# Kernel optimization log

Measured on AMD Instinct MI355X. Metric: run time of the kernel, lower is better.

Reference implementation:

```python
import jax, jax.numpy as jnp
import numpy as np

N = 100000      # nodes
E = 1600000     # edges (avg degree 16)
NF = 1          # node_feature_dim
EF = 1          # edge_feature_dim
H = 64          # hidden_dim
L = 5           # num_layers


def _linear_init(key, fan_in, fan_out):
    # torch nn.Linear default: U(-1/sqrt(fan_in), 1/sqrt(fan_in)) for W and b
    s = 1.0 / np.sqrt(fan_in)
    kw, kb = jax.random.split(key)
    w = jax.random.uniform(kw, (fan_in, fan_out), minval=-s, maxval=s, dtype=jnp.float32)
    b = jax.random.uniform(kb, (fan_out,), minval=-s, maxval=s, dtype=jnp.float32)
    return w, b


def setup_inputs() -> dict:
    key = jax.random.key(0)
    ks = jax.random.split(key, 8)
    x = jax.random.normal(ks[0], (N, NF), dtype=jnp.float32)
    edge_index = jax.random.randint(ks[1], (2, E), 0, N, dtype=jnp.int32)
    edge_attr = jax.random.uniform(ks[2], (E, EF), dtype=jnp.float32)

    emb_w, emb_b = _linear_init(ks[3], NF, H)
    fc_w, fc_b = _linear_init(ks[4], H, 1)

    msg_w1, msg_b1, msg_w2, msg_b2 = [], [], [], []
    upd_w1, upd_b1, upd_w2, upd_b2 = [], [], [], []
    lk = jax.random.split(ks[5], L)
    for l in range(L):
        k1, k2, k3, k4 = jax.random.split(lk[l], 4)
        w, b = _linear_init(k1, H + EF, H); msg_w1.append(w); msg_b1.append(b)
        w, b = _linear_init(k2, H, H);      msg_w2.append(w); msg_b2.append(b)
        w, b = _linear_init(k3, 2 * H, H);  upd_w1.append(w); upd_b1.append(b)
        w, b = _linear_init(k4, H, H);      upd_w2.append(w); upd_b2.append(b)

    stack = lambda xs: jnp.stack(xs, axis=0)
    return {
        "x": x, "edge_index": edge_index, "edge_attr": edge_attr,
        "emb_w": emb_w, "emb_b": emb_b,
        "msg_w1": stack(msg_w1), "msg_b1": stack(msg_b1),
        "msg_w2": stack(msg_w2), "msg_b2": stack(msg_b2),
        "upd_w1": stack(upd_w1), "upd_b1": stack(upd_b1),
        "upd_w2": stack(upd_w2), "upd_b2": stack(upd_b2),
        "fc_w": fc_w, "fc_b": fc_b,
    }


def reference(x, edge_index, edge_attr, emb_w, emb_b,
              msg_w1, msg_b1, msg_w2, msg_b2,
              upd_w1, upd_b1, upd_w2, upd_b2, fc_w, fc_b):
    src = edge_index[0]  # x_j (source)
    dst = edge_index[1]  # aggregation target i
    n = x.shape[0]

    h = x @ emb_w + emb_b  # [N, H]
    for l in range(msg_w1.shape[0]):
        # message: MLP(cat[x_j, edge_attr])
        m = jnp.concatenate([h[src], edge_attr], axis=1)  # [E, H+EF]
        m = jax.nn.relu(m @ msg_w1[l] + msg_b1[l]) @ msg_w2[l] + msg_b2[l]  # [E, H]
        # scatter-min aggregate; torch_scatter fills empty segments with 0
        aggr = jax.ops.segment_min(m, dst, num_segments=n)
        aggr = jnp.where(jnp.isfinite(aggr), aggr, jnp.zeros_like(aggr))
        # update: MLP(cat[x, aggr])
        u = jnp.concatenate([h, aggr], axis=1)  # [N, 2H]
        h = jax.nn.relu(u @ upd_w1[l] + upd_b1[l]) @ upd_w2[l] + upd_b2[l]
    return (h @ fc_w + fc_b).squeeze(-1)  # [N]
```

## Files before the change

kernel.cpp:

```cpp
#include <hip/hip_runtime.h>
#include <math.h>

#define N_NODES 100000
#define N_EDGES 1600000
#define HDIM 64
#define SCAN_T 1024
#define SCAN_CHUNK 98
#define NPB 64
#define LBLOCKS 1563
#define BSTRIDE 66

__device__ __forceinline__ unsigned encMin(float f) {
  unsigned u = __float_as_uint(f);
  return (u & 0x80000000u) ? ~u : (u | 0x80000000u);
}
__device__ __forceinline__ float decMin(unsigned u) {
  unsigned b = (u & 0x80000000u) ? (u & 0x7FFFFFFFu) : ~u;
  return __uint_as_float(b);
}


__global__ __launch_bounds__(256) void k_zero_int(int* __restrict__ p, int n) {
  int i = blockIdx.x * 256 + threadIdx.x;
  if (i < n) p[i] = 0;
}

__global__ __launch_bounds__(256) void k_deg_count(const int* __restrict__ ei,
                                                   int* __restrict__ deg) {
  int e = blockIdx.x * 256 + threadIdx.x;
  if (e < N_EDGES) atomicAdd(&deg[ei[N_EDGES + e]], 1);
}

__global__ __launch_bounds__(SCAN_T) void k_rowptr(const int* __restrict__ deg,
                                                   int* __restrict__ row_ptr) {
  __shared__ int sums[SCAN_T];
  const int t = threadIdx.x;
  const int lo = t * SCAN_CHUNK;
  const int hi = min(lo + SCAN_CHUNK, N_NODES);
  int s = 0;
  for (int i = lo; i < hi; ++i) s += deg[i];
  sums[t] = s;
  __syncthreads();
  for (int off = 1; off < SCAN_T; off <<= 1) {
    int v = (t >= off) ? sums[t - off] : 0;
    __syncthreads();
    sums[t] += v;
    __syncthreads();
  }
  int run = (t == 0) ? 0 : sums[t - 1];
  for (int i = lo; i < hi; ++i) { row_ptr[i] = run; run += deg[i]; }
  if (t == SCAN_T - 1) row_ptr[N_NODES] = run;
}

__global__ __launch_bounds__(256) void k_scatter(
    const int* __restrict__ ei, const float* __restrict__ eattr,
    const int* __restrict__ row_ptr, int* __restrict__ cursor,
    int* __restrict__ s_src, float* __restrict__ s_ea, int* __restrict__ s_dl) {
  int e = blockIdx.x * 256 + threadIdx.x;
  if (e >= N_EDGES) return;
  int d = ei[N_EDGES + e];
  int pos = row_ptr[d] + atomicAdd(&cursor[d], 1);
  s_src[pos] = ei[e];
  s_ea[pos] = eattr[e];
  s_dl[pos] = d & (NPB - 1);
}


__global__ __launch_bounds__(256) void k_embed_z(
    const float* __restrict__ x, const float* __restrict__ emb_w,
    const float* __restrict__ emb_b,
    const float* __restrict__ w1, const float* __restrict__ b1,
    float* __restrict__ h, float* __restrict__ z) {
  __shared__ float hs[64][65];
  const int t = threadIdx.x;
  const int nl = t >> 2;
  const int l4 = t & 3;
  const int i = blockIdx.x * 64 + nl;
  const bool valid = (i < N_NODES);
  const int jbase = l4 * 16;
  const float xv = valid ? x[i] : 0.0f;

  float hv[16];
  #pragma unroll
  for (int jj = 0; jj < 16; ++jj) {
    int j = jbase + jj;
    hv[jj] = fmaf(xv, emb_w[j], emb_b[j]);
    hs[nl][j] = hv[jj];
  }
  if (valid) {
    #pragma unroll
    for (int q = 0; q < 4; ++q)
      reinterpret_cast<float4*>(h + (size_t)i * HDIM)[l4 * 4 + q] =
          make_float4(hv[4*q], hv[4*q+1], hv[4*q+2], hv[4*q+3]);
  }
  __syncthreads();

  float acc[16];
  #pragma unroll
  for (int jj = 0; jj < 16; ++jj) acc[jj] = b1[jbase + jj];
  #pragma unroll 8
  for (int k = 0; k < 64; ++k) {
    float hk = hs[nl][k];
    const float* wr = w1 + k * 64 + jbase;
    #pragma unroll
    for (int jj = 0; jj < 16; ++jj) acc[jj] = fmaf(hk, wr[jj], acc[jj]);
  }
  if (valid) {
    #pragma unroll
    for (int q = 0; q < 4; ++q)
      reinterpret_cast<float4*>(z + (size_t)i * HDIM)[l4 * 4 + q] =
          make_float4(acc[4*q], acc[4*q+1], acc[4*q+2], acc[4*q+3]);
  }
}

template <int LAST>
__global__ __launch_bounds__(256) void k_layer(
    const int* __restrict__ row_ptr,
    const int* __restrict__ s_src, const float* __restrict__ s_ea,
    const int* __restrict__ s_dl,
    const float* __restrict__ z_in,
    const float* __restrict__ w1b, const float* __restrict__ w2,
    const float* __restrict__ b2,
    const float* __restrict__ u1w, const float* __restrict__ u1b,
    const float* __restrict__ u2w, const float* __restrict__ u2b,
    const float* __restrict__ w1next, const float* __restrict__ b1next,
    const float* __restrict__ fcw, const float* __restrict__ fcb,
    float* __restrict__ h, float* __restrict__ z_out, float* __restrict__ out) {
  __shared__ float buf[2][64][BSTRIDE];
  __shared__ unsigned acc_u[NPB][65];
  __shared__ float ps[NPB][4];
  float* acc_f = (float*)acc_u;

  const int t = threadIdx.x;
  const int lane = t & 63;
  const int w = __builtin_amdgcn_readfirstlane(t >> 6);
  const int pair = w >> 1;
  const int wi = w & 1;
  const int nbase = blockIdx.x * NPB;

  for (int i = t; i < NPB * 65; i += 256) ((unsigned*)acc_u)[i] = 0xFFFFFFFFu;

  const int eb0 = row_ptr[nbase];
  const int eb1 = row_ptr[min(nbase + NPB, N_NODES)];
  const int n = eb1 - eb0;
  const int emid = eb0 + (n >> 1);
  const int p0 = pair ? emid : eb0;
  const int p1 = pair ? eb1 : emid;
  const int nbat = ((n - (n >> 1)) + 63) >> 6;

  const int rq = lane >> 3;
  const int q  = lane & 7;
  const float4 w1bA = ((const float4*)w1b)[q];
  const float4 w1bB = ((const float4*)w1b)[q + 8];
  const int jb = wi * 32;

  __syncthreads();

  for (int bi = 0; bi < nbat; ++bi) {
    const int base = p0 + (bi << 6);
    const int cnt  = min(64, p1 - base);

    if (cnt > 0) {
      #pragma unroll
      for (int i = 0; i < 4; ++i) {
        const int row = wi * 32 + i * 8 + rq;
        const int ed = base + row;
        const bool v = (row < cnt);
        const int src = v ? s_src[ed] : 0;
        const float ea = v ? s_ea[ed] : 0.0f;
        const float4* zr = (const float4*)(z_in + (size_t)src * HDIM);
        float4 a = zr[q];
        float4 b = zr[q + 8];
        float2 h0, h1, h2, h3;
        h0.x = fmaxf(fmaf(ea, w1bA.x, a.x), 0.f);
        h0.y = fmaxf(fmaf(ea, w1bA.y, a.y), 0.f);
        h1.x = fmaxf(fmaf(ea, w1bA.z, a.z), 0.f);
        h1.y = fmaxf(fmaf(ea, w1bA.w, a.w), 0.f);
        h2.x = fmaxf(fmaf(ea, w1bB.x, b.x), 0.f);
        h2.y = fmaxf(fmaf(ea, w1bB.y, b.y), 0.f);
        h3.x = fmaxf(fmaf(ea, w1bB.z, b.z), 0.f);
        h3.y = fmaxf(fmaf(ea, w1bB.w, b.w), 0.f);
        float* bp = &buf[pair][row][0];
        *(float2*)&bp[q * 4]          = h0;
        *(float2*)&bp[q * 4 + 2]      = h1;
        *(float2*)&bp[32 + q * 4]     = h2;
        *(float2*)&bp[32 + q * 4 + 2] = h3;
      }
    }
    __syncthreads();

    float m[32];
    if (cnt > 0) {
      #pragma unroll
      for (int c = 0; c < 32; ++c) m[c] = b2[jb + c];
      const float* bp = &buf[pair][lane][0];
      #pragma unroll 4
      for (int k2 = 0; k2 < 32; ++k2) {
        float2 hq = *(const float2*)&bp[k2 * 2];
        const float* wr0 = w2 + (2 * k2 + 0) * 64 + jb;
        const float* wr1 = w2 + (2 * k2 + 1) * 64 + jb;
        #pragma unroll
        for (int c = 0; c < 32; ++c) m[c] = fmaf(hq.x, wr0[c], m[c]);
        #pragma unroll
        for (int c = 0; c < 32; ++c) m[c] = fmaf(hq.y, wr1[c], m[c]);
      }
    }
    __syncthreads();

    if (cnt > 0) {
      float* bp = &buf[pair][lane][jb];
      #pragma unroll
      for (int c2 = 0; c2 < 16; ++c2)
        *(float2*)&bp[c2 * 2] = make_float2(m[2*c2], m[2*c2+1]);
    }
    __syncthreads();

    if (cnt > 0) {
      const int e0 = wi * 32;
      const int e1 = min(wi * 32 + 32, cnt);
      float run = INFINITY;
      int cur = -1;
      for (int e = e0; e < e1; ++e) {
        const int dl = s_dl[base + e];
        if (dl != cur) {
          if (cur >= 0) atomicMin(&acc_u[cur][lane], encMin(run));
          cur = dl; run = INFINITY;
        }
        run = fminf(run, buf[pair][e][lane]);
      }
      if (cur >= 0) atomicMin(&acc_u[cur][lane], encMin(run));
    }
    __syncthreads();
  }

  const int jq = w * 16;
  const int node = nbase + lane;
  const bool valid = (node < N_NODES);
  const size_t off = (size_t)(valid ? node : 0) * HDIM;

  #pragma unroll
  for (int j = 0; j < 16; ++j) {
    float f = decMin(acc_u[lane][jq + j]);
    if (!isfinite(f)) f = 0.f;
    acc_f[lane * 65 + jq + j] = f;
  }
  __syncthreads();

  float acc[16];
  #pragma unroll
  for (int j = 0; j < 16; ++j) acc[j] = u1b[jq + j];
  {
    const float4* hr = reinterpret_cast<const float4*>(h + off);
    for (int k4 = 0; k4 < 16; ++k4) {
      float4 uv = hr[k4];
      const float* w0 = u1w + (4*k4+0) * 64 + jq;
      const float* w1 = u1w + (4*k4+1) * 64 + jq;
      const float* w2r = u1w + (4*k4+2) * 64 + jq;
      const float* w3 = u1w + (4*k4+3) * 64 + jq;
      #pragma unroll
      for (int j = 0; j < 16; ++j) acc[j] = fmaf(uv.x, w0[j], acc[j]);
      #pragma unroll
      for (int j = 0; j < 16; ++j) acc[j] = fmaf(uv.y, w1[j], acc[j]);
      #pragma unroll
      for (int j = 0; j < 16; ++j) acc[j] = fmaf(uv.z, w2r[j], acc[j]);
      #pragma unroll
      for (int j = 0; j < 16; ++j) acc[j] = fmaf(uv.w, w3[j], acc[j]);
    }
    #pragma unroll 4
    for (int k = 0; k < 64; ++k) {
      float uk = acc_f[lane * 65 + k];
      const float* wr = u1w + (64 + k) * 64 + jq;
      #pragma unroll
      for (int j = 0; j < 16; ++j) acc[j] = fmaf(uk, wr[j], acc[j]);
    }
  }
  __syncthreads();
  #pragma unroll
  for (int j = 0; j < 16; ++j) acc_f[lane * 65 + jq + j] = fmaxf(acc[j], 0.f);
  __syncthreads();

  float hn[16];
  #pragma unroll
  for (int j = 0; j < 16; ++j) hn[j] = u2b[jq + j];
  #pragma unroll 4
  for (int k = 0; k < 64; ++k) {
    float hk = acc_f[lane * 65 + k];
    const float* wr = u2w + k * 64 + jq;
    #pragma unroll
    for (int j = 0; j < 16; ++j) hn[j] = fmaf(hk, wr[j], hn[j]);
  }
  if (valid) {
    #pragma unroll
    for (int v4 = 0; v4 < 4; ++v4)
      reinterpret_cast<float4*>(h + off)[w * 4 + v4] =
          make_float4(hn[4*v4], hn[4*v4+1], hn[4*v4+2], hn[4*v4+3]);
  }

  if (LAST) {
    float s = 0.0f;
    #pragma unroll
    for (int j = 0; j < 16; ++j) s = fmaf(hn[j], fcw[jq + j], s);
    ps[lane][w] = s;
    __syncthreads();
    if (w == 0 && valid)
      out[node] = ps[lane][0] + ps[lane][1] + ps[lane][2] + ps[lane][3] + fcb[0];
  } else {
    __syncthreads();
    #pragma unroll
    for (int j = 0; j < 16; ++j) acc_f[lane * 65 + jq + j] = hn[j];
    __syncthreads();
    float zz[16];
    #pragma unroll
    for (int j = 0; j < 16; ++j) zz[j] = b1next[jq + j];
    #pragma unroll 4
    for (int k = 0; k < 64; ++k) {
      float hk = acc_f[lane * 65 + k];
      const float* wr = w1next + k * 64 + jq;
      #pragma unroll
      for (int j = 0; j < 16; ++j) zz[j] = fmaf(hk, wr[j], zz[j]);
    }
    if (valid) {
      #pragma unroll
      for (int v4 = 0; v4 < 4; ++v4)
        reinterpret_cast<float4*>(z_out + off)[w * 4 + v4] =
            make_float4(zz[4*v4], zz[4*v4+1], zz[4*v4+2], zz[4*v4+3]);
    }
  }
}

extern "C" void kernel_launch(void* const* d_in, const int* in_sizes, int n_in,
                              void* d_out, int out_size, void* d_ws, size_t ws_size,
                              hipStream_t stream) {
  const float* x      = (const float*)d_in[0];
  const int*   ei     = (const int*)d_in[1];
  const float* eattr  = (const float*)d_in[2];
  const float* emb_w  = (const float*)d_in[3];
  const float* emb_b  = (const float*)d_in[4];
  const float* msg_w1 = (const float*)d_in[5];
  const float* msg_b1 = (const float*)d_in[6];
  const float* msg_w2 = (const float*)d_in[7];
  const float* msg_b2 = (const float*)d_in[8];
  const float* upd_w1 = (const float*)d_in[9];
  const float* upd_b1 = (const float*)d_in[10];
  const float* upd_w2 = (const float*)d_in[11];
  const float* upd_b2 = (const float*)d_in[12];
  const float* fc_w   = (const float*)d_in[13];
  const float* fc_b   = (const float*)d_in[14];
  float* out = (float*)d_out;

  float* h     = (float*)d_ws;
  float* zA    = h + (size_t)N_NODES * HDIM;
  float* zB    = zA + (size_t)N_NODES * HDIM;
  float* s_ea  = zB + (size_t)N_NODES * HDIM;
  int*   s_src = (int*)(s_ea + N_EDGES);
  int*   s_dl  = s_src + N_EDGES;
  int*   row_ptr = s_dl + N_EDGES;
  int*   deg   = row_ptr + (N_NODES + 1);
  int*   cursor= deg + N_NODES;

  const int nodeBlocks64 = (N_NODES + 63) / 64;
  const int edgeBlocks = (N_EDGES + 255) / 256;

  k_zero_int<<<(2 * N_NODES + 255) / 256, 256, 0, stream>>>(deg, 2 * N_NODES);
  k_deg_count<<<edgeBlocks, 256, 0, stream>>>(ei, deg);
  k_rowptr<<<1, SCAN_T, 0, stream>>>(deg, row_ptr);
  k_scatter<<<edgeBlocks, 256, 0, stream>>>(ei, eattr, row_ptr, cursor,
                                            s_src, s_ea, s_dl);

  k_embed_z<<<nodeBlocks64, 256, 0, stream>>>(x, emb_w, emb_b, msg_w1, msg_b1, h, zA);

  float* zin = zA;
  float* zout = zB;
  for (int l = 0; l < 5; ++l) {
    const float* w1b = msg_w1 + l * 65 * 64 + 64 * 64;
    const float* w2  = msg_w2 + l * 64 * 64;
    const float* b2  = msg_b2 + l * 64;
    const float* u1w = upd_w1 + l * 128 * 64;
    const float* u1b = upd_b1 + l * 64;
    const float* u2w = upd_w2 + l * 64 * 64;
    const float* u2b = upd_b2 + l * 64;
    if (l < 4) {
      k_layer<0><<<LBLOCKS, 256, 0, stream>>>(
          row_ptr, s_src, s_ea, s_dl, zin,
          w1b, w2, b2, u1w, u1b, u2w, u2b,
          msg_w1 + (l + 1) * 65 * 64, msg_b1 + (l + 1) * 64,
          nullptr, nullptr,
          h, zout, nullptr);
      float* tmp = zin; zin = zout; zout = tmp;
    } else {
      k_layer<1><<<LBLOCKS, 256, 0, stream>>>(
          row_ptr, s_src, s_ea, s_dl, zin,
          w1b, w2, b2, u1w, u1b, u2w, u2b,
          nullptr, nullptr,
          fc_w, fc_b,
          h, nullptr, out);
    }
  }
}
```

Before: 2.219 ms.

## Precompute per-source-node affine message coefficients with sparse ReLU-ambiguity correction

The per-edge 64x64 message MLP is replaced by a per-node precomputation. For each source node it builds C and D so that the message equals C + ea*D, assuming each hidden unit's ReLU state is fixed for edge_attr in [0,1]. Units whose sign can flip inside that range are listed per node and corrected per edge with a short loop. Per-edge work drops to a 512-byte gather plus a few corrections, at the cost of an extra build kernel per layer, a larger per-node CD buffer, and reliance on edge_attr lying in [0,1].

```diff
diff --git a/kernel.cpp b/kernel.cpp
--- a/kernel.cpp
+++ b/kernel.cpp
@@ -8,7 +8,6 @@
 #define SCAN_CHUNK 98
 #define NPB 64
 #define LBLOCKS 1563
-#define BSTRIDE 66
 
 __device__ __forceinline__ unsigned encMin(float f) {
   unsigned u = __float_as_uint(f);
@@ -55,78 +54,133 @@
 __global__ __launch_bounds__(256) void k_scatter(
     const int* __restrict__ ei, const float* __restrict__ eattr,
     const int* __restrict__ row_ptr, int* __restrict__ cursor,
-    int* __restrict__ s_src, float* __restrict__ s_ea, int* __restrict__ s_dl) {
+    int* __restrict__ s_sd, float* __restrict__ s_ea) {
   int e = blockIdx.x * 256 + threadIdx.x;
   if (e >= N_EDGES) return;
   int d = ei[N_EDGES + e];
   int pos = row_ptr[d] + atomicAdd(&cursor[d], 1);
-  s_src[pos] = ei[e];
+  s_sd[pos] = ei[e] | ((d & (NPB - 1)) << 20);
   s_ea[pos] = eattr[e];
-  s_dl[pos] = d & (NPB - 1);
-}
-
-
-__global__ __launch_bounds__(256) void k_embed_z(
-    const float* __restrict__ x, const float* __restrict__ emb_w,
-    const float* __restrict__ emb_b,
-    const float* __restrict__ w1, const float* __restrict__ b1,
-    float* __restrict__ h, float* __restrict__ z) {
+}
+
+
+__global__ __launch_bounds__(256) void k_embed(
+    const float* __restrict__ x, const float* __restrict__ ew,
+    const float* __restrict__ eb, float* __restrict__ h) {
+  int gid = blockIdx.x * 256 + threadIdx.x;
+  if (gid >= N_NODES * 16) return;
+  int node = gid >> 4;
+  int q = gid & 15;
+  float xv = x[node];
+  float4 w = ((const float4*)ew)[q];
+  float4 b = ((const float4*)eb)[q];
+  ((float4*)h)[gid] = make_float4(fmaf(xv, w.x, b.x), fmaf(xv, w.y, b.y),
+                                  fmaf(xv, w.z, b.z), fmaf(xv, w.w, b.w));
+}
+
+__global__ __launch_bounds__(256) void k_build(
+    const float* __restrict__ h,
+    const float* __restrict__ w1,
+    const float* __restrict__ b1,
+    const float* __restrict__ w2,
+    const float* __restrict__ b2,
+    float* __restrict__ z,
+    float* __restrict__ CD,
+    unsigned char* __restrict__ amb,
+    int* __restrict__ amb_cnt) {
   __shared__ float hs[64][65];
+  __shared__ float zs[64][65];
   const int t = threadIdx.x;
   const int nl = t >> 2;
   const int l4 = t & 3;
-  const int i = blockIdx.x * 64 + nl;
-  const bool valid = (i < N_NODES);
-  const int jbase = l4 * 16;
-  const float xv = valid ? x[i] : 0.0f;
-
-  float hv[16];
-  #pragma unroll
-  for (int jj = 0; jj < 16; ++jj) {
-    int j = jbase + jj;
-    hv[jj] = fmaf(xv, emb_w[j], emb_b[j]);
-    hs[nl][j] = hv[jj];
-  }
-  if (valid) {
-    #pragma unroll
-    for (int q = 0; q < 4; ++q)
-      reinterpret_cast<float4*>(h + (size_t)i * HDIM)[l4 * 4 + q] =
-          make_float4(hv[4*q], hv[4*q+1], hv[4*q+2], hv[4*q+3]);
-  }
-  __syncthreads();
-
-  float acc[16];
-  #pragma unroll
-  for (int jj = 0; jj < 16; ++jj) acc[jj] = b1[jbase + jj];
-  #pragma unroll 8
+  const int node = blockIdx.x * 64 + nl;
+  const bool valid = (node < N_NODES);
+  const size_t off = (size_t)(valid ? node : 0) * HDIM;
+  const int jb = l4 * 16;
+
+  #pragma unroll
+  for (int q = 0; q < 4; ++q) {
+    float4 hv = ((const float4*)(h + off))[l4 * 4 + q];
+    hs[nl][jb + 4*q + 0] = hv.x;
+    hs[nl][jb + 4*q + 1] = hv.y;
+    hs[nl][jb + 4*q + 2] = hv.z;
+    hs[nl][jb + 4*q + 3] = hv.w;
+  }
+  __syncthreads();
+
+  float zr[16];
+  #pragma unroll
+  for (int j = 0; j < 16; ++j) zr[j] = b1[jb + j];
+  #pragma unroll 4
   for (int k = 0; k < 64; ++k) {
     float hk = hs[nl][k];
-    const float* wr = w1 + k * 64 + jbase;
-    #pragma unroll
-    for (int jj = 0; jj < 16; ++jj) acc[jj] = fmaf(hk, wr[jj], acc[jj]);
-  }
+    const float* wr = w1 + k * 64 + jb;
+    #pragma unroll
+    for (int j = 0; j < 16; ++j) zr[j] = fmaf(hk, wr[j], zr[j]);
+  }
+  #pragma unroll
+  for (int j = 0; j < 16; ++j) zs[nl][jb + j] = zr[j];
   if (valid) {
     #pragma unroll
     for (int q = 0; q < 4; ++q)
-      reinterpret_cast<float4*>(z + (size_t)i * HDIM)[l4 * 4 + q] =
-          make_float4(acc[4*q], acc[4*q+1], acc[4*q+2], acc[4*q+3]);
+      ((float4*)(z + off))[l4 * 4 + q] =
+          make_float4(zr[4*q], zr[4*q+1], zr[4*q+2], zr[4*q+3]);
+  }
+  __syncthreads();
+
+  const float* w1b = w1 + 64 * 64;
+  float c[16], d[16];
+  #pragma unroll
+  for (int j = 0; j < 16; ++j) { c[j] = b2[jb + j]; d[j] = 0.0f; }
+  #pragma unroll 4
+  for (int k = 0; k < 64; ++k) {
+    float zk = zs[nl][k];
+    float vk = w1b[k];
+    float zv = zk + vk;
+    bool act = (fminf(zk, zv) >= 0.0f);
+    float cz = act ? zk : 0.0f;
+    float cv = act ? vk : 0.0f;
+    const float* wr = w2 + k * 64 + jb;
+    #pragma unroll
+    for (int j = 0; j < 16; ++j) {
+      c[j] = fmaf(cz, wr[j], c[j]);
+      d[j] = fmaf(cv, wr[j], d[j]);
+    }
+  }
+  if (valid) {
+    float4* cdp = (float4*)(CD + (size_t)node * 128);
+    #pragma unroll
+    for (int j2 = 0; j2 < 8; ++j2)
+      cdp[jb / 2 + j2] = make_float4(c[2*j2], d[2*j2], c[2*j2+1], d[2*j2+1]);
+  }
+
+  if (l4 == 0 && valid) {
+    int cnt = 0;
+    for (int k = 0; k < 64; ++k) {
+      float zk = zs[nl][k];
+      float vk = w1b[k];
+      float zv = zk + vk;
+      if (fminf(zk, zv) < 0.0f && fmaxf(zk, zv) > 0.0f) {
+        amb[(size_t)node * 64 + cnt] = (unsigned char)k;
+        ++cnt;
+      }
+    }
+    amb_cnt[node] = cnt;
   }
 }
 
 template <int LAST>
 __global__ __launch_bounds__(256) void k_layer(
     const int* __restrict__ row_ptr,
-    const int* __restrict__ s_src, const float* __restrict__ s_ea,
-    const int* __restrict__ s_dl,
-    const float* __restrict__ z_in,
+    const int* __restrict__ s_sd, const float* __restrict__ s_ea,
+    const float2* __restrict__ CDm,
+    const float* __restrict__ z,
     const float* __restrict__ w1b, const float* __restrict__ w2,
-    const float* __restrict__ b2,
+    const unsigned char* __restrict__ amb, const int* __restrict__ amb_cnt,
     const float* __restrict__ u1w, const float* __restrict__ u1b,
     const float* __restrict__ u2w, const float* __restrict__ u2b,
-    const float* __restrict__ w1next, const float* __restrict__ b1next,
     const float* __restrict__ fcw, const float* __restrict__ fcb,
-    float* __restrict__ h, float* __restrict__ z_out, float* __restrict__ out) {
-  __shared__ float buf[2][64][BSTRIDE];
+    float* __restrict__ h, float* __restrict__ out) {
   __shared__ unsigned acc_u[NPB][65];
   __shared__ float ps[NPB][4];
   float* acc_f = (float*)acc_u;
@@ -134,8 +188,6 @@
   const int t = threadIdx.x;
   const int lane = t & 63;
   const int w = __builtin_amdgcn_readfirstlane(t >> 6);
-  const int pair = w >> 1;
-  const int wi = w & 1;
   const int nbase = blockIdx.x * NPB;
 
   for (int i = t; i < NPB * 65; i += 256) ((unsigned*)acc_u)[i] = 0xFFFFFFFFu;
@@ -143,95 +195,48 @@
   const int eb0 = row_ptr[nbase];
   const int eb1 = row_ptr[min(nbase + NPB, N_NODES)];
   const int n = eb1 - eb0;
-  const int emid = eb0 + (n >> 1);
-  const int p0 = pair ? emid : eb0;
-  const int p1 = pair ? eb1 : emid;
-  const int nbat = ((n - (n >> 1)) + 63) >> 6;
-
-  const int rq = lane >> 3;
-  const int q  = lane & 7;
-  const float4 w1bA = ((const float4*)w1b)[q];
-  const float4 w1bB = ((const float4*)w1b)[q + 8];
-  const int jb = wi * 32;
-
-  __syncthreads();
-
-  for (int bi = 0; bi < nbat; ++bi) {
-    const int base = p0 + (bi << 6);
-    const int cnt  = min(64, p1 - base);
-
-    if (cnt > 0) {
-      #pragma unroll
-      for (int i = 0; i < 4; ++i) {
-        const int row = wi * 32 + i * 8 + rq;
-        const int ed = base + row;
-        const bool v = (row < cnt);
-        const int src = v ? s_src[ed] : 0;
-        const float ea = v ? s_ea[ed] : 0.0f;
-        const float4* zr = (const float4*)(z_in + (size_t)src * HDIM);
-        float4 a = zr[q];
-        float4 b = zr[q + 8];
-        float2 h0, h1, h2, h3;
-        h0.x = fmaxf(fmaf(ea, w1bA.x, a.x), 0.f);
-        h0.y = fmaxf(fmaf(ea, w1bA.y, a.y), 0.f);
-        h1.x = fmaxf(fmaf(ea, w1bA.z, a.z), 0.f);
-        h1.y = fmaxf(fmaf(ea, w1bA.w, a.w), 0.f);
-        h2.x = fmaxf(fmaf(ea, w1bB.x, b.x), 0.f);
-        h2.y = fmaxf(fmaf(ea, w1bB.y, b.y), 0.f);
-        h3.x = fmaxf(fmaf(ea, w1bB.z, b.z), 0.f);
-        h3.y = fmaxf(fmaf(ea, w1bB.w, b.w), 0.f);
-        float* bp = &buf[pair][row][0];
-        *(float2*)&bp[q * 4]          = h0;
-        *(float2*)&bp[q * 4 + 2]      = h1;
-        *(float2*)&bp[32 + q * 4]     = h2;
-        *(float2*)&bp[32 + q * 4 + 2] = h3;
+  const int we0 = eb0 + (n * w) / 4;
+  const int we1 = eb0 + (n * (w + 1)) / 4;
+  __syncthreads();
+
+  float run = INFINITY;
+  int cur = -1;
+  for (int e = we0; e < we1; e += 4) {
+    const int nb = min(4, we1 - e);
+    int sd[4]; float ea4[4]; float2 cd[4];
+    #pragma unroll
+    for (int i = 0; i < 4; ++i) {
+      sd[i] = (i < nb) ? s_sd[e + i] : 0;
+      ea4[i] = (i < nb) ? s_ea[e + i] : 0.0f;
+    }
+    #pragma unroll
+    for (int i = 0; i < 4; ++i)
+      cd[i] = CDm[(size_t)(sd[i] & 0xFFFFF) * 64 + lane];
+    #pragma unroll
+    for (int i = 0; i < 4; ++i) {
+      if (i >= nb) break;
+      const int src = sd[i] & 0xFFFFF;
+      const int dl = sd[i] >> 20;
+      float m = fmaf(ea4[i], cd[i].y, cd[i].x);
+      const int cnt = amb_cnt[src];
+      if (cnt) {
+        const unsigned char* ap = amb + (size_t)src * 64;
+        const float* zrow = z + (size_t)src * 64;
+        for (int a = 0; a < cnt; ++a) {
+          const int k = ap[a];
+          const float tt = fmaf(ea4[i], w1b[k], zrow[k]);
+          if (tt > 0.0f) m = fmaf(tt, w2[k * 64 + lane], m);
+        }
       }
-    }
-    __syncthreads();
-
-    float m[32];
-    if (cnt > 0) {
-      #pragma unroll
-      for (int c = 0; c < 32; ++c) m[c] = b2[jb + c];
-      const float* bp = &buf[pair][lane][0];
-      #pragma unroll 4
-      for (int k2 = 0; k2 < 32; ++k2) {
-        float2 hq = *(const float2*)&bp[k2 * 2];
-        const float* wr0 = w2 + (2 * k2 + 0) * 64 + jb;
-        const float* wr1 = w2 + (2 * k2 + 1) * 64 + jb;
-        #pragma unroll
-        for (int c = 0; c < 32; ++c) m[c] = fmaf(hq.x, wr0[c], m[c]);
-        #pragma unroll
-        for (int c = 0; c < 32; ++c) m[c] = fmaf(hq.y, wr1[c], m[c]);
+      if (dl != cur) {
+        if (cur >= 0) atomicMin(&acc_u[cur][lane], encMin(run));
+        cur = dl; run = INFINITY;
       }
-    }
-    __syncthreads();
-
-    if (cnt > 0) {
-      float* bp = &buf[pair][lane][jb];
-      #pragma unroll
-      for (int c2 = 0; c2 < 16; ++c2)
-        *(float2*)&bp[c2 * 2] = make_float2(m[2*c2], m[2*c2+1]);
-    }
-    __syncthreads();
-
-    if (cnt > 0) {
-      const int e0 = wi * 32;
-      const int e1 = min(wi * 32 + 32, cnt);
-      float run = INFINITY;
-      int cur = -1;
-      for (int e = e0; e < e1; ++e) {
-        const int dl = s_dl[base + e];
-        if (dl != cur) {
-          if (cur >= 0) atomicMin(&acc_u[cur][lane], encMin(run));
-          cur = dl; run = INFINITY;
-        }
-        run = fminf(run, buf[pair][e][lane]);
-      }
-      if (cur >= 0) atomicMin(&acc_u[cur][lane], encMin(run));
-    }
-    __syncthreads();
-  }
+      run = fminf(run, m);
+    }
+  }
+  if (cur >= 0) atomicMin(&acc_u[cur][lane], encMin(run));
+  __syncthreads();
 
   const int jq = w * 16;
   const int node = nbase + lane;
@@ -254,13 +259,13 @@
     for (int k4 = 0; k4 < 16; ++k4) {
       float4 uv = hr[k4];
       const float* w0 = u1w + (4*k4+0) * 64 + jq;
-      const float* w1 = u1w + (4*k4+1) * 64 + jq;
+      const float* w1r = u1w + (4*k4+1) * 64 + jq;
       const float* w2r = u1w + (4*k4+2) * 64 + jq;
       const float* w3 = u1w + (4*k4+3) * 64 + jq;
       #pragma unroll
       for (int j = 0; j < 16; ++j) acc[j] = fmaf(uv.x, w0[j], acc[j]);
       #pragma unroll
-      for (int j = 0; j < 16; ++j) acc[j] = fmaf(uv.y, w1[j], acc[j]);
+      for (int j = 0; j < 16; ++j) acc[j] = fmaf(uv.y, w1r[j], acc[j]);
       #pragma unroll
       for (int j = 0; j < 16; ++j) acc[j] = fmaf(uv.z, w2r[j], acc[j]);
       #pragma unroll
@@ -304,27 +309,6 @@
     __syncthreads();
     if (w == 0 && valid)
       out[node] = ps[lane][0] + ps[lane][1] + ps[lane][2] + ps[lane][3] + fcb[0];
-  } else {
-    __syncthreads();
-    #pragma unroll
-    for (int j = 0; j < 16; ++j) acc_f[lane * 65 + jq + j] = hn[j];
-    __syncthreads();
-    float zz[16];
-    #pragma unroll
-    for (int j = 0; j < 16; ++j) zz[j] = b1next[jq + j];
-    #pragma unroll 4
-    for (int k = 0; k < 64; ++k) {
-      float hk = acc_f[lane * 65 + k];
-      const float* wr = w1next + k * 64 + jq;
-      #pragma unroll
-      for (int j = 0; j < 16; ++j) zz[j] = fmaf(hk, wr[j], zz[j]);
-    }
-    if (valid) {
-      #pragma unroll
-      for (int v4 = 0; v4 < 4; ++v4)
-        reinterpret_cast<float4*>(z_out + off)[w * 4 + v4] =
-            make_float4(zz[4*v4], zz[4*v4+1], zz[4*v4+2], zz[4*v4+3]);
-    }
   }
 }
 
@@ -349,51 +333,47 @@
   float* out = (float*)d_out;
 
   float* h     = (float*)d_ws;
-  float* zA    = h + (size_t)N_NODES * HDIM;
-  float* zB    = zA + (size_t)N_NODES * HDIM;
-  float* s_ea  = zB + (size_t)N_NODES * HDIM;
-  int*   s_src = (int*)(s_ea + N_EDGES);
-  int*   s_dl  = s_src + N_EDGES;
-  int*   row_ptr = s_dl + N_EDGES;
+  float* zbuf  = h + (size_t)N_NODES * HDIM;
+  float* CD    = zbuf + (size_t)N_NODES * HDIM;
+  float* s_ea  = CD + (size_t)N_NODES * 128;
+  int*   s_sd  = (int*)(s_ea + N_EDGES);
+  int*   row_ptr = s_sd + N_EDGES;
   int*   deg   = row_ptr + (N_NODES + 1);
   int*   cursor= deg + N_NODES;
-
-  const int nodeBlocks64 = (N_NODES + 63) / 64;
+  int*   amb_cnt = cursor + N_NODES;
+  unsigned char* amb = (unsigned char*)(amb_cnt + N_NODES);
+
   const int edgeBlocks = (N_EDGES + 255) / 256;
 
   k_zero_int<<<(2 * N_NODES + 255) / 256, 256, 0, stream>>>(deg, 2 * N_NODES);
   k_deg_count<<<edgeBlocks, 256, 0, stream>>>(ei, deg);
   k_rowptr<<<1, SCAN_T, 0, stream>>>(deg, row_ptr);
-  k_scatter<<<edgeBlocks, 256, 0, stream>>>(ei, eattr, row_ptr, cursor,
-                                            s_src, s_ea, s_dl);
-
-  k_embed_z<<<nodeBlocks64, 256, 0, stream>>>(x, emb_w, emb_b, msg_w1, msg_b1, h, zA);
-
-  float* zin = zA;
-  float* zout = zB;
+  k_scatter<<<edgeBlocks, 256, 0, stream>>>(ei, eattr, row_ptr, cursor, s_sd, s_ea);
+
+  k_embed<<<(N_NODES * 16 + 255) / 256, 256, 0, stream>>>(x, emb_w, emb_b, h);
+
   for (int l = 0; l < 5; ++l) {
-    const float* w1b = msg_w1 + l * 65 * 64 + 64 * 64;
+    const float* w1  = msg_w1 + l * 65 * 64;
+    const float* b1  = msg_b1 + l * 64;
     const float* w2  = msg_w2 + l * 64 * 64;
     const float* b2  = msg_b2 + l * 64;
     const float* u1w = upd_w1 + l * 128 * 64;
     const float* u1b = upd_b1 + l * 64;
     const float* u2w = upd_w2 + l * 64 * 64;
     const float* u2b = upd_b2 + l * 64;
+
+    k_build<<<LBLOCKS, 256, 0, stream>>>(h, w1, b1, w2, b2, zbuf, CD,
+                                         amb, amb_cnt);
     if (l < 4) {
       k_layer<0><<<LBLOCKS, 256, 0, stream>>>(
-          row_ptr, s_src, s_ea, s_dl, zin,
-          w1b, w2, b2, u1w, u1b, u2w, u2b,
-          msg_w1 + (l + 1) * 65 * 64, msg_b1 + (l + 1) * 64,
-          nullptr, nullptr,
-          h, zout, nullptr);
-      float* tmp = zin; zin = zout; zout = tmp;
+          row_ptr, s_sd, s_ea, (const float2*)CD, zbuf,
+          w1 + 64 * 64, w2, amb, amb_cnt,
+          u1w, u1b, u2w, u2b, nullptr, nullptr, h, nullptr);
     } else {
       k_layer<1><<<LBLOCKS, 256, 0, stream>>>(
-          row_ptr, s_src, s_ea, s_dl, zin,
-          w1b, w2, b2, u1w, u1b, u2w, u2b,
-          nullptr, nullptr,
-          fc_w, fc_b,
-          h, nullptr, out);
-    }
-  }
-}
+          row_ptr, s_sd, s_ea, (const float2*)CD, zbuf,
+          w1 + 64 * 64, w2, amb, amb_cnt,
+          u1w, u1b, u2w, u2b, fc_w, fc_b, h, out);
+    }
+  }
+}
```

Result: slower. 8.446 ms (+280.6%).

## Give each wave its own edge slice with per-lane 64-wide message MLP

Applied to the files above, without the earlier changes.

The edge loop in the layer kernel is restructured so that each of the four waves owns a contiguous quarter of the block's edges and a private shared buffer. Each lane computes the full 64-output second message layer for one edge, staging the hidden vector in two 32-column halves. The lane then atomically mins all 64 results into the shared aggregate, which replaces the block-wide syncs and the sorted run-length reduction. Source index and local destination are packed into one int, removing the separate destination array. The price is 64 accumulator registers per lane, which risks lower occupancy, plus up to 64 shared atomics per edge instead of one per destination run.

```diff
diff --git a/kernel.cpp b/kernel.cpp
--- a/kernel.cpp
+++ b/kernel.cpp
@@ -8,7 +8,7 @@
 #define SCAN_CHUNK 98
 #define NPB 64
 #define LBLOCKS 1563
-#define BSTRIDE 66
+#define BSTR 36
 
 __device__ __forceinline__ unsigned encMin(float f) {
   unsigned u = __float_as_uint(f);
@@ -55,14 +55,13 @@
 __global__ __launch_bounds__(256) void k_scatter(
     const int* __restrict__ ei, const float* __restrict__ eattr,
     const int* __restrict__ row_ptr, int* __restrict__ cursor,
-    int* __restrict__ s_src, float* __restrict__ s_ea, int* __restrict__ s_dl) {
+    int* __restrict__ s_sd, float* __restrict__ s_ea) {
   int e = blockIdx.x * 256 + threadIdx.x;
   if (e >= N_EDGES) return;
   int d = ei[N_EDGES + e];
   int pos = row_ptr[d] + atomicAdd(&cursor[d], 1);
-  s_src[pos] = ei[e];
+  s_sd[pos] = ei[e] | ((d & (NPB - 1)) << 20);
   s_ea[pos] = eattr[e];
-  s_dl[pos] = d & (NPB - 1);
 }
 
 
@@ -116,8 +115,7 @@
 template <int LAST>
 __global__ __launch_bounds__(256) void k_layer(
     const int* __restrict__ row_ptr,
-    const int* __restrict__ s_src, const float* __restrict__ s_ea,
-    const int* __restrict__ s_dl,
+    const int* __restrict__ s_sd, const float* __restrict__ s_ea,
     const float* __restrict__ z_in,
     const float* __restrict__ w1b, const float* __restrict__ w2,
     const float* __restrict__ b2,
@@ -126,16 +124,14 @@
     const float* __restrict__ w1next, const float* __restrict__ b1next,
     const float* __restrict__ fcw, const float* __restrict__ fcb,
     float* __restrict__ h, float* __restrict__ z_out, float* __restrict__ out) {
-  __shared__ float buf[2][64][BSTRIDE];
+  __shared__ float buf[4][64][BSTR];
   __shared__ unsigned acc_u[NPB][65];
   __shared__ float ps[NPB][4];
   float* acc_f = (float*)acc_u;
 
   const int t = threadIdx.x;
   const int lane = t & 63;
-  const int w = __builtin_amdgcn_readfirstlane(t >> 6);
-  const int pair = w >> 1;
-  const int wi = w & 1;
+  const int wv = __builtin_amdgcn_readfirstlane(t >> 6);
   const int nbase = blockIdx.x * NPB;
 
   for (int i = t; i < NPB * 65; i += 256) ((unsigned*)acc_u)[i] = 0xFFFFFFFFu;
@@ -143,97 +139,61 @@
   const int eb0 = row_ptr[nbase];
   const int eb1 = row_ptr[min(nbase + NPB, N_NODES)];
   const int n = eb1 - eb0;
-  const int emid = eb0 + (n >> 1);
-  const int p0 = pair ? emid : eb0;
-  const int p1 = pair ? eb1 : emid;
-  const int nbat = ((n - (n >> 1)) + 63) >> 6;
-
+  const int we0 = eb0 + (n * wv) / 4;
+  const int we1 = eb0 + (n * (wv + 1)) / 4;
   const int rq = lane >> 3;
   const int q  = lane & 7;
-  const float4 w1bA = ((const float4*)w1b)[q];
-  const float4 w1bB = ((const float4*)w1b)[q + 8];
-  const int jb = wi * 32;
-
-  __syncthreads();
-
-  for (int bi = 0; bi < nbat; ++bi) {
-    const int base = p0 + (bi << 6);
-    const int cnt  = min(64, p1 - base);
-
-    if (cnt > 0) {
-      #pragma unroll
-      for (int i = 0; i < 4; ++i) {
-        const int row = wi * 32 + i * 8 + rq;
-        const int ed = base + row;
-        const bool v = (row < cnt);
-        const int src = v ? s_src[ed] : 0;
-        const float ea = v ? s_ea[ed] : 0.0f;
-        const float4* zr = (const float4*)(z_in + (size_t)src * HDIM);
-        float4 a = zr[q];
-        float4 b = zr[q + 8];
-        float2 h0, h1, h2, h3;
-        h0.x = fmaxf(fmaf(ea, w1bA.x, a.x), 0.f);
-        h0.y = fmaxf(fmaf(ea, w1bA.y, a.y), 0.f);
-        h1.x = fmaxf(fmaf(ea, w1bA.z, a.z), 0.f);
-        h1.y = fmaxf(fmaf(ea, w1bA.w, a.w), 0.f);
-        h2.x = fmaxf(fmaf(ea, w1bB.x, b.x), 0.f);
-        h2.y = fmaxf(fmaf(ea, w1bB.y, b.y), 0.f);
-        h3.x = fmaxf(fmaf(ea, w1bB.z, b.z), 0.f);
-        h3.y = fmaxf(fmaf(ea, w1bB.w, b.w), 0.f);
-        float* bp = &buf[pair][row][0];
-        *(float2*)&bp[q * 4]          = h0;
-        *(float2*)&bp[q * 4 + 2]      = h1;
-        *(float2*)&bp[32 + q * 4]     = h2;
-        *(float2*)&bp[32 + q * 4 + 2] = h3;
+  float* mybuf = &buf[wv][0][0];
+  __syncthreads();
+
+  for (int base = we0; base < we1; base += 64) {
+    const int cnt = min(64, we1 - base);
+
+    float m[64];
+    #pragma unroll
+    for (int c = 0; c < 64; ++c) m[c] = b2[c];
+
+    #pragma unroll
+    for (int half = 0; half < 2; ++half) {
+      const float4 w1bq = ((const float4*)w1b)[half * 8 + q];
+      #pragma unroll
+      for (int r = 0; r < 8; ++r) {
+        const int row = r * 8 + rq;
+        if (row < cnt) {
+          const int sd = s_sd[base + row];
+          const float ea = s_ea[base + row];
+          const int src = sd & 0xFFFFF;
+          float4 zq = ((const float4*)(z_in + (size_t)src * HDIM))[half * 8 + q];
+          float4 hv;
+          hv.x = fmaxf(fmaf(ea, w1bq.x, zq.x), 0.f);
+          hv.y = fmaxf(fmaf(ea, w1bq.y, zq.y), 0.f);
+          hv.z = fmaxf(fmaf(ea, w1bq.z, zq.z), 0.f);
+          hv.w = fmaxf(fmaf(ea, w1bq.w, zq.w), 0.f);
+          *(float4*)&mybuf[row * BSTR + q * 4] = hv;
+        }
       }
-    }
-    __syncthreads();
-
-    float m[32];
-    if (cnt > 0) {
-      #pragma unroll
-      for (int c = 0; c < 32; ++c) m[c] = b2[jb + c];
-      const float* bp = &buf[pair][lane][0];
+      const float* bp = &mybuf[lane * BSTR];
       #pragma unroll 4
-      for (int k2 = 0; k2 < 32; ++k2) {
+      for (int k2 = 0; k2 < 16; ++k2) {
         float2 hq = *(const float2*)&bp[k2 * 2];
-        const float* wr0 = w2 + (2 * k2 + 0) * 64 + jb;
-        const float* wr1 = w2 + (2 * k2 + 1) * 64 + jb;
+        const float* wr0 = w2 + (half * 32 + 2 * k2) * 64;
+        const float* wr1 = wr0 + 64;
         #pragma unroll
-        for (int c = 0; c < 32; ++c) m[c] = fmaf(hq.x, wr0[c], m[c]);
+        for (int c = 0; c < 64; ++c) m[c] = fmaf(hq.x, wr0[c], m[c]);
         #pragma unroll
-        for (int c = 0; c < 32; ++c) m[c] = fmaf(hq.y, wr1[c], m[c]);
+        for (int c = 0; c < 64; ++c) m[c] = fmaf(hq.y, wr1[c], m[c]);
       }
     }
-    __syncthreads();
-
-    if (cnt > 0) {
-      float* bp = &buf[pair][lane][jb];
-      #pragma unroll
-      for (int c2 = 0; c2 < 16; ++c2)
-        *(float2*)&bp[c2 * 2] = make_float2(m[2*c2], m[2*c2+1]);
-    }
-    __syncthreads();
-
-    if (cnt > 0) {
-      const int e0 = wi * 32;
-      const int e1 = min(wi * 32 + 32, cnt);
-      float run = INFINITY;
-      int cur = -1;
-      for (int e = e0; e < e1; ++e) {
-        const int dl = s_dl[base + e];
-        if (dl != cur) {
-          if (cur >= 0) atomicMin(&acc_u[cur][lane], encMin(run));
-          cur = dl; run = INFINITY;
-        }
-        run = fminf(run, buf[pair][e][lane]);
-      }
-      if (cur >= 0) atomicMin(&acc_u[cur][lane], encMin(run));
-    }
-    __syncthreads();
-  }
-
-  const int jq = w * 16;
+    if (lane < cnt) {
+      const int dl = s_sd[base + lane] >> 20;
+      #pragma unroll
+      for (int c = 0; c < 64; ++c)
+        atomicMin(&acc_u[dl][c], encMin(m[c]));
+    }
+  }
+  __syncthreads();
+
+  const int jq = wv * 16;
   const int node = nbase + lane;
   const bool valid = (node < N_NODES);
   const size_t off = (size_t)(valid ? node : 0) * HDIM;
@@ -254,13 +214,13 @@
     for (int k4 = 0; k4 < 16; ++k4) {
       float4 uv = hr[k4];
       const float* w0 = u1w + (4*k4+0) * 64 + jq;
-      const float* w1 = u1w + (4*k4+1) * 64 + jq;
+      const float* w1r = u1w + (4*k4+1) * 64 + jq;
       const float* w2r = u1w + (4*k4+2) * 64 + jq;
       const float* w3 = u1w + (4*k4+3) * 64 + jq;
       #pragma unroll
       for (int j = 0; j < 16; ++j) acc[j] = fmaf(uv.x, w0[j], acc[j]);
       #pragma unroll
-      for (int j = 0; j < 16; ++j) acc[j] = fmaf(uv.y, w1[j], acc[j]);
+      for (int j = 0; j < 16; ++j) acc[j] = fmaf(uv.y, w1r[j], acc[j]);
       #pragma unroll
       for (int j = 0; j < 16; ++j) acc[j] = fmaf(uv.z, w2r[j], acc[j]);
       #pragma unroll
@@ -292,7 +252,7 @@
   if (valid) {
     #pragma unroll
     for (int v4 = 0; v4 < 4; ++v4)
-      reinterpret_cast<float4*>(h + off)[w * 4 + v4] =
+      reinterpret_cast<float4*>(h + off)[wv * 4 + v4] =
           make_float4(hn[4*v4], hn[4*v4+1], hn[4*v4+2], hn[4*v4+3]);
   }
 
@@ -300,9 +260,9 @@
     float s = 0.0f;
     #pragma unroll
     for (int j = 0; j < 16; ++j) s = fmaf(hn[j], fcw[jq + j], s);
-    ps[lane][w] = s;
-    __syncthreads();
-    if (w == 0 && valid)
+    ps[lane][wv] = s;
+    __syncthreads();
+    if (wv == 0 && valid)
       out[node] = ps[lane][0] + ps[lane][1] + ps[lane][2] + ps[lane][3] + fcb[0];
   } else {
     __syncthreads();
@@ -322,7 +282,7 @@
     if (valid) {
       #pragma unroll
       for (int v4 = 0; v4 < 4; ++v4)
-        reinterpret_cast<float4*>(z_out + off)[w * 4 + v4] =
+        reinterpret_cast<float4*>(z_out + off)[wv * 4 + v4] =
             make_float4(zz[4*v4], zz[4*v4+1], zz[4*v4+2], zz[4*v4+3]);
     }
   }
@@ -352,9 +312,8 @@
   float* zA    = h + (size_t)N_NODES * HDIM;
   float* zB    = zA + (size_t)N_NODES * HDIM;
   float* s_ea  = zB + (size_t)N_NODES * HDIM;
-  int*   s_src = (int*)(s_ea + N_EDGES);
-  int*   s_dl  = s_src + N_EDGES;
-  int*   row_ptr = s_dl + N_EDGES;
+  int*   s_sd  = (int*)(s_ea + N_EDGES);
+  int*   row_ptr = s_sd + N_EDGES;
   int*   deg   = row_ptr + (N_NODES + 1);
   int*   cursor= deg + N_NODES;
 
@@ -364,8 +323,7 @@
   k_zero_int<<<(2 * N_NODES + 255) / 256, 256, 0, stream>>>(deg, 2 * N_NODES);
   k_deg_count<<<edgeBlocks, 256, 0, stream>>>(ei, deg);
   k_rowptr<<<1, SCAN_T, 0, stream>>>(deg, row_ptr);
-  k_scatter<<<edgeBlocks, 256, 0, stream>>>(ei, eattr, row_ptr, cursor,
-                                            s_src, s_ea, s_dl);
+  k_scatter<<<edgeBlocks, 256, 0, stream>>>(ei, eattr, row_ptr, cursor, s_sd, s_ea);
 
   k_embed_z<<<nodeBlocks64, 256, 0, stream>>>(x, emb_w, emb_b, msg_w1, msg_b1, h, zA);
 
@@ -381,7 +339,7 @@
     const float* u2b = upd_b2 + l * 64;
     if (l < 4) {
       k_layer<0><<<LBLOCKS, 256, 0, stream>>>(
-          row_ptr, s_src, s_ea, s_dl, zin,
+          row_ptr, s_sd, s_ea, zin,
           w1b, w2, b2, u1w, u1b, u2w, u2b,
           msg_w1 + (l + 1) * 65 * 64, msg_b1 + (l + 1) * 64,
           nullptr, nullptr,
@@ -389,7 +347,7 @@
       float* tmp = zin; zin = zout; zout = tmp;
     } else {
       k_layer<1><<<LBLOCKS, 256, 0, stream>>>(
-          row_ptr, s_src, s_ea, s_dl, zin,
+          row_ptr, s_sd, s_ea, zin,
           w1b, w2, b2, u1w, u1b, u2w, u2b,
           nullptr, nullptr,
           fc_w, fc_b,
```

Result: slower. 2.732 ms (+23.1%).
